# Kernel tuning notes

Hardware: AMD Instinct MI355X
Metric: run time of the kernel (lower is better)

The kernel has to match this reference:

```python
import jax, jax.numpy as jnp
import numpy as np

N = 50000  # nodes


def gcn_layer(x, src, dst, W, b):
    """DGL GraphConv with norm='both': D_in^{-1/2} A^T D_out^{-1/2} x W + b."""
    E = src.shape[0]
    ones = jnp.ones((E,), dtype=x.dtype)
    deg_out = jax.ops.segment_sum(ones, src, num_segments=N)  # out-degree of src nodes
    deg_in = jax.ops.segment_sum(ones, dst, num_segments=N)   # in-degree of dst nodes
    norm_src = jax.lax.rsqrt(jnp.maximum(deg_out, 1.0))
    norm_dst = jax.lax.rsqrt(jnp.maximum(deg_in, 1.0))
    h = x * norm_src[:, None]
    agg = jax.ops.segment_sum(h[src], dst, num_segments=N)  # [N, in_dim]
    return (agg @ W) * norm_dst[:, None] + b


def encoder(feat, src, dst, W1, b1, W2, b2):
    h = jax.nn.relu(gcn_layer(feat, src, dst, W1, b1))
    h = jax.nn.relu(gcn_layer(h, src, dst, W2, b2))
    return h


def proj(h, fc1_W, fc1_b, fc2_W, fc2_b):
    z = jax.nn.elu(h @ fc1_W + fc1_b)
    return z @ fc2_W + fc2_b


def setup_inputs() -> dict:
    key = jax.random.key(0)
    ks = jax.random.split(key, 12)
    in_dim, hid, out_dim, E = 128, 128, 128, 800000
    inp = {
        "feat1": jax.random.normal(ks[0], (N, in_dim), dtype=jnp.float32),
        "feat2": jax.random.normal(ks[1], (N, in_dim), dtype=jnp.float32),
        "edge_index1": jax.random.randint(ks[2], (2, E), 0, N),
        "edge_index2": jax.random.randint(ks[3], (2, E), 0, N),
        # GraphConv weights: in_dim -> 2*hid -> hid
        "conv1_W": jax.random.normal(ks[4], (in_dim, 2 * hid), dtype=jnp.float32) * 0.05,
        "conv1_b": jnp.zeros((2 * hid,), dtype=jnp.float32),
        "conv2_W": jax.random.normal(ks[5], (2 * hid, hid), dtype=jnp.float32) * 0.05,
        "conv2_b": jnp.zeros((hid,), dtype=jnp.float32),
        # MLP proj: fc1 hid->out, fc2 out->hid
        "fc1_W": jax.random.normal(ks[6], (hid, out_dim), dtype=jnp.float32) * 0.05,
        "fc1_b": jnp.zeros((out_dim,), dtype=jnp.float32),
        "fc2_W": jax.random.normal(ks[7], (out_dim, hid), dtype=jnp.float32) * 0.05,
        "fc2_b": jnp.zeros((hid,), dtype=jnp.float32),
    }
    return inp


def reference(feat1, feat2, edge_index1, edge_index2,
              conv1_W, conv1_b, conv2_W, conv2_b,
              fc1_W, fc1_b, fc2_W, fc2_b):
    h1 = encoder(feat1, edge_index1[0], edge_index1[1], conv1_W, conv1_b, conv2_W, conv2_b)
    h2 = encoder(feat2, edge_index2[0], edge_index2[1], conv1_W, conv1_b, conv2_W, conv2_b)
    z1 = proj(h1, fc1_W, fc1_b, fc2_W, fc2_b)
    z2 = proj(h2, fc1_W, fc1_b, fc2_W, fc2_b)
    return (z1, z2)
```

## Files before the change

### kernel.cpp

```cpp
#include <hip/hip_runtime.h>
#include <math.h>

#define NDIM 128
#define H2   256
#define MAXG 2
#define TPE  8192
#define NBKMAX 512

typedef __attribute__((ext_vector_type(8))) short bf16x8;
typedef __attribute__((ext_vector_type(4))) float f32x4;

__device__ __forceinline__ unsigned short f2bf(float f) {
    unsigned int u = __float_as_uint(f);
    u += 0x7fffu + ((u >> 16) & 1u);
    return (unsigned short)(u >> 16);
}
__device__ __forceinline__ float bf2f(unsigned short h) {
    return __uint_as_float(((unsigned int)h) << 16);
}
__device__ __forceinline__ void split2(float f, unsigned short& h, unsigned short& l) {
    h = f2bf(f);
    l = f2bf(f - bf2f(h));
}

__device__ __forceinline__ void gload16(const unsigned short* g, unsigned short* l) {
    __builtin_amdgcn_global_load_lds(
        (const __attribute__((address_space(1))) unsigned int*)g,
        (__attribute__((address_space(3))) unsigned int*)l, 16, 0, 0);
}

struct BinArgs {
    const int* src[MAXG]; const int* dst[MAXG];
    int* histD[MAXG]; int* histS[MAXG];
    int* totD[MAXG];  int* baseD[MAXG];
    int* totS[MAXG];  int* baseS[MAXG];
    unsigned int* pairs[MAXG];
    unsigned short* srcS[MAXG];
    int E[MAXG]; int NBK; int NT; int n;
};

__global__ __launch_bounds__(256) void binA(BinArgs a) {
    __shared__ int cntD[NBKMAX], cntS[NBKMAX];
    int g = blockIdx.y, t = blockIdx.x, tid = threadIdx.x;
    for (int b = tid; b < NBKMAX; b += 256) { cntD[b] = 0; cntS[b] = 0; }
    __syncthreads();
    int E = a.E[g];
    int base = t * TPE;
#pragma unroll
    for (int k = 0; k < TPE / 256; ++k) {
        int e = base + k * 256 + tid;
        if (e < E) {
            atomicAdd(&cntD[a.dst[g][e] >> 7], 1);
            atomicAdd(&cntS[a.src[g][e] >> 7], 1);
        }
    }
    __syncthreads();
    for (int b = tid; b < a.NBK; b += 256) {
        a.histD[g][t * a.NBK + b] = cntD[b];
        a.histS[g][t * a.NBK + b] = cntS[b];
    }
}

__global__ __launch_bounds__(512) void binB(BinArgs a) {
    int g = blockIdx.y, side = blockIdx.z;
    int* hist = side ? a.histS[g] : a.histD[g];
    int* tot  = side ? a.totS[g]  : a.totD[g];
    int* base = side ? a.baseS[g] : a.baseD[g];
    __shared__ int s[512];
    int b = threadIdx.x;
    int v = 0;
    if (b < a.NBK)
        for (int t = 0; t < a.NT; ++t) v += hist[t * a.NBK + b];
    s[b] = v;
    __syncthreads();
    for (int off = 1; off < 512; off <<= 1) {
        int u = (b >= off) ? s[b - off] : 0;
        __syncthreads();
        s[b] += u;
        __syncthreads();
    }
    int excl = s[b] - v;
    if (b < a.NBK) {
        tot[b] = v;
        base[b] = excl;
        int run = excl;
        for (int t = 0; t < a.NT; ++t) {
            int h = hist[t * a.NBK + b];
            hist[t * a.NBK + b] = run;
            run += h;
        }
    }
}

__global__ __launch_bounds__(256) void binC(BinArgs a) {
    __shared__ int offD[NBKMAX], offS[NBKMAX];
    int g = blockIdx.y, t = blockIdx.x, tid = threadIdx.x;
    for (int b = tid; b < a.NBK; b += 256) {
        offD[b] = a.histD[g][t * a.NBK + b];
        offS[b] = a.histS[g][t * a.NBK + b];
    }
    __syncthreads();
    int E = a.E[g];
    int base = t * TPE;
    unsigned int* pairs = a.pairs[g];
    unsigned short* ss = a.srcS[g];
#pragma unroll
    for (int k = 0; k < TPE / 256; ++k) {
        int e = base + k * 256 + tid;
        if (e < E) {
            int s = a.src[g][e], d = a.dst[g][e];
            int pos = atomicAdd(&offD[d >> 7], 1);
            pairs[pos] = ((unsigned int)(d & 127) << 16) | (unsigned int)s;
            int posS = atomicAdd(&offS[s >> 7], 1);
            ss[posS] = (unsigned short)s;
        }
    }
}

struct FinArgs {
    const unsigned int* pairs[MAXG];
    const unsigned short* srcS[MAXG];
    const int* totD[MAXG]; const int* baseD[MAXG];
    const int* totS[MAXG]; const int* baseS[MAXG];
    int* row_ptr[MAXG]; int* row_end[MAXG];
    unsigned short* edge_srt[MAXG];
    float* ns[MAXG]; float* nd[MAXG];
    int n;
};

__global__ __launch_bounds__(256) void finalize(FinArgs a) {
    __shared__ int cnt[128], hist[128], scn[128], cur[128];
    int g = blockIdx.y, bkt = blockIdx.x, tid = threadIdx.x;
    if (tid < 128) { cnt[tid] = 0; hist[tid] = 0; }
    __syncthreads();
    {
        int base = a.baseS[g][bkt], tot = a.totS[g][bkt];
        const unsigned short* ss = a.srcS[g];
        for (int i = tid; i < tot; i += 256)
            atomicAdd(&cnt[ss[base + i] & 127], 1);
    }
    int cntE = a.totD[g][bkt], base = a.baseD[g][bkt];
    const unsigned int* pp = a.pairs[g] + base;
    for (int i = tid; i < cntE; i += 256)
        atomicAdd(&hist[pp[i] >> 16], 1);
    __syncthreads();
    if (tid < 128) {
        int node = bkt * 128 + tid;
        if (node < a.n) {
            int c = cnt[tid];
            a.ns[g][node] = rsqrtf((float)(c > 1 ? c : 1));
        }
        scn[tid] = hist[tid];
    }
    __syncthreads();
    for (int off = 1; off < 128; off <<= 1) {
        int v = (tid < 128 && tid >= off) ? scn[tid - off] : 0;
        __syncthreads();
        if (tid < 128) scn[tid] += v;
        __syncthreads();
    }
    if (tid < 128) {
        int incl = scn[tid];
        int h = hist[tid];
        cur[tid] = incl - h;
        int node = bkt * 128 + tid;
        if (node < a.n) {
            a.row_ptr[g][node] = base + incl - h;
            a.row_end[g][node] = base + incl;
            a.nd[g][node] = rsqrtf((float)(h > 1 ? h : 1));
        }
    }
    __syncthreads();
    for (int i = tid; i < cntE; i += 256) {
        unsigned int p = pp[i];
        int pos = atomicAdd(&cur[p >> 16], 1);
        a.edge_srt[g][base + pos] = (unsigned short)(p & 0xFFFF);
    }
}

struct GatherArgs {
    const float* X[MAXG];
    const int* row_ptr[MAXG]; const int* row_end[MAXG];
    const unsigned short* edge_src[MAXG];
    const float* nd[MAXG];
    const float* sns[MAXG];
    unsigned short* outH[MAXG]; unsigned short* outL[MAXG];
    const float* bias; int use_nd; int use_sns; int n;
};

__global__ __launch_bounds__(256) void gather_split_b(GatherArgs a) {
    int g = blockIdx.y;
    int half = threadIdx.x >> 5;
    int lane = threadIdx.x & 31;
    int r = blockIdx.x * 8 + half;
    if (r >= a.n) return;
    int j = a.row_ptr[g][r];
    int end = a.row_end[g][r];
    const unsigned short* ep = a.edge_src[g];
    const float* X = a.X[g];
    const float* sns = a.sns[g];
    int base = lane * 4;
    float4 acc = make_float4(0.f, 0.f, 0.f, 0.f);
    if (a.use_sns) {
        for (; j + 3 < end; j += 4) {
            int s0 = ep[j], s1 = ep[j + 1], s2 = ep[j + 2], s3 = ep[j + 3];
            float n0 = sns[s0], n1 = sns[s1], n2 = sns[s2], n3 = sns[s3];
            float4 v0 = *(const float4*)(X + (size_t)s0 * NDIM + base);
            float4 v1 = *(const float4*)(X + (size_t)s1 * NDIM + base);
            float4 v2 = *(const float4*)(X + (size_t)s2 * NDIM + base);
            float4 v3 = *(const float4*)(X + (size_t)s3 * NDIM + base);
            acc.x = fmaf(v0.x, n0, fmaf(v1.x, n1, fmaf(v2.x, n2, fmaf(v3.x, n3, acc.x))));
            acc.y = fmaf(v0.y, n0, fmaf(v1.y, n1, fmaf(v2.y, n2, fmaf(v3.y, n3, acc.y))));
            acc.z = fmaf(v0.z, n0, fmaf(v1.z, n1, fmaf(v2.z, n2, fmaf(v3.z, n3, acc.z))));
            acc.w = fmaf(v0.w, n0, fmaf(v1.w, n1, fmaf(v2.w, n2, fmaf(v3.w, n3, acc.w))));
        }
        for (; j < end; ++j) {
            int s0 = ep[j];
            float n0 = sns[s0];
            float4 v0 = *(const float4*)(X + (size_t)s0 * NDIM + base);
            acc.x = fmaf(v0.x, n0, acc.x); acc.y = fmaf(v0.y, n0, acc.y);
            acc.z = fmaf(v0.z, n0, acc.z); acc.w = fmaf(v0.w, n0, acc.w);
        }
    } else {
        for (; j + 3 < end; j += 4) {
            int s0 = ep[j], s1 = ep[j + 1], s2 = ep[j + 2], s3 = ep[j + 3];
            float4 v0 = *(const float4*)(X + (size_t)s0 * NDIM + base);
            float4 v1 = *(const float4*)(X + (size_t)s1 * NDIM + base);
            float4 v2 = *(const float4*)(X + (size_t)s2 * NDIM + base);
            float4 v3 = *(const float4*)(X + (size_t)s3 * NDIM + base);
            acc.x += v0.x + v1.x + v2.x + v3.x;
            acc.y += v0.y + v1.y + v2.y + v3.y;
            acc.z += v0.z + v1.z + v2.z + v3.z;
            acc.w += v0.w + v1.w + v2.w + v3.w;
        }
        for (; j < end; ++j) {
            int s0 = ep[j];
            float4 v0 = *(const float4*)(X + (size_t)s0 * NDIM + base);
            acc.x += v0.x; acc.y += v0.y; acc.z += v0.z; acc.w += v0.w;
        }
    }
    float v[4] = {acc.x, acc.y, acc.z, acc.w};
    if (a.use_nd) {
        float s = a.nd[g][r];
#pragma unroll
        for (int i = 0; i < 4; ++i)
            v[i] = fmaxf(v[i] * s + a.bias[base + i], 0.f);
    }
    unsigned short h[4], l[4];
#pragma unroll
    for (int i = 0; i < 4; ++i) split2(v[i], h[i], l[i]);
    *(ushort4*)(a.outH[g] + (size_t)r * NDIM + base) = make_ushort4(h[0], h[1], h[2], h[3]);
    *(ushort4*)(a.outL[g] + (size_t)r * NDIM + base) = make_ushort4(l[0], l[1], l[2], l[3]);
}

__global__ void wprep_all(const float* __restrict__ W1, const float* __restrict__ W2,
                          const float* __restrict__ F1, const float* __restrict__ F2,
                          unsigned short* __restrict__ W1h, unsigned short* __restrict__ W1l,
                          unsigned short* __restrict__ W2h, unsigned short* __restrict__ W2l,
                          unsigned short* __restrict__ F1h, unsigned short* __restrict__ F1l,
                          unsigned short* __restrict__ F2h, unsigned short* __restrict__ F2l) {
    int i = blockIdx.x * 256 + threadIdx.x;
    const float* Wsrc; unsigned short *Hd, *Ld; int K, Nc, idx;
    if (i < 32768)       { Wsrc = W1; Hd = W1h; Ld = W1l; K = 128; Nc = 256; idx = i; }
    else if (i < 65536)  { Wsrc = W2; Hd = W2h; Ld = W2l; K = 256; Nc = 128; idx = i - 32768; }
    else if (i < 81920)  { Wsrc = F1; Hd = F1h; Ld = F1l; K = 128; Nc = 128; idx = i - 65536; }
    else                 { Wsrc = F2; Hd = F2h; Ld = F2l; K = 128; Nc = 128; idx = i - 81920; }
    int k = idx / Nc, n = idx % Nc;
    unsigned short h, l;
    split2(Wsrc[idx], h, l);
    Hd[n * K + k] = h;
    Ld[n * K + k] = l;
}

struct FusedArgs {
    const unsigned short* Ah[MAXG]; const unsigned short* Al[MAXG];
    const unsigned short* B1h; const unsigned short* B1l;
    const unsigned short* B2h; const unsigned short* B2l;
    const float* rs1[MAXG];
    const float* rs2[MAXG];
    const float* b1v;
    const float* b2v;
    float* C[MAXG];
    int M, has_rs1, has_rs2, has_b1, has_b2;
};

template <int K1, int N1, int ACT1, int ROWS>
__global__ __launch_bounds__(256) void fused_gemm2(FusedArgs a) {
    constexpr int IR   = ROWS / 16;
    constexpr int SH_A = ROWS * K1;
    constexpr int SH_X = ROWS * N1;
    constexpr int SH   = (2 * SH_A > 2 * SH_X) ? 2 * SH_A : 2 * SH_X;
    __shared__ __align__(16) unsigned short S[SH];
    unsigned short* As_h = S;
    unsigned short* As_l = S + SH_A;
    unsigned short* Xs_h = S;
    unsigned short* Xs_l = S + SH_X;

    int g = blockIdx.y;
    const unsigned short* __restrict__ Ah_g = a.Ah[g];
    const unsigned short* __restrict__ Al_g = a.Al[g];
    const unsigned short* __restrict__ B1h = a.B1h;
    const unsigned short* __restrict__ B1l = a.B1l;
    const unsigned short* __restrict__ B2h = a.B2h;
    const unsigned short* __restrict__ B2l = a.B2l;

    int tid  = threadIdx.x;
    int wave = tid >> 6, lane = tid & 63;
    int quad = lane >> 4, l16 = lane & 15;
    int rowBase = blockIdx.x * ROWS;
    int M = a.M;

    constexpr int J1  = N1 / 64;
    constexpr int KT1 = K1 / 32;
    constexpr int KT2 = N1 / 32;
    int wcol1 = wave * (N1 / 4);
    int wcol2 = wave * 32;

    size_t b1off[J1];
#pragma unroll
    for (int j = 0; j < J1; ++j)
        b1off[j] = (size_t)(wcol1 + j * 16 + l16) * K1 + quad * 8;
    size_t b2off[2];
#pragma unroll
    for (int j = 0; j < 2; ++j)
        b2off[j] = (size_t)(wcol2 + j * 16 + l16) * N1 + quad * 8;

    auto loadB1 = [&](int kt, bf16x8 (&bh)[J1], bf16x8 (&bl)[J1]) {
#pragma unroll
        for (int j = 0; j < J1; ++j) {
            bh[j] = *(const bf16x8*)(B1h + b1off[j] + kt * 32);
            bl[j] = *(const bf16x8*)(B1l + b1off[j] + kt * 32);
        }
    };
    auto loadB2 = [&](int kt, bf16x8 (&bh)[2], bf16x8 (&bl)[2]) {
#pragma unroll
        for (int j = 0; j < 2; ++j) {
            bh[j] = *(const bf16x8*)(B2h + b2off[j] + kt * 32);
            bl[j] = *(const bf16x8*)(B2l + b2off[j] + kt * 32);
        }
    };

    bf16x8 b1hA[J1], b1lA[J1], b1hB[J1], b1lB[J1];
    loadB1(0, b1hA, b1lA);

    constexpr int CPR = K1 / 8;
#pragma unroll
    for (int it = 0; it < (ROWS * CPR) / 256; ++it) {
        int waveChunk = it * 256 + wave * 64;
        int cl   = waveChunk + lane;
        int row  = cl / CPR;
        int cpos = cl % CPR;
        int oc   = cpos ^ (row & 7);
        int grow = rowBase + row; if (grow > M - 1) grow = M - 1;
        gload16(Ah_g + (size_t)grow * K1 + oc * 8, As_h + (size_t)waveChunk * 8);
        gload16(Al_g + (size_t)grow * K1 + oc * 8, As_l + (size_t)waveChunk * 8);
    }
    __syncthreads();

    f32x4 acc1[IR][J1] = {};
    auto stepP1 = [&](int kt, bf16x8 (&bh)[J1], bf16x8 (&bl)[J1]) {
        bf16x8 af[IR], alf[IR];
#pragma unroll
        for (int i = 0; i < IR; ++i) {
            int r  = i * 16 + l16;
            int sc = (kt * 4 + quad) ^ (r & 7);
            af[i]  = *(const bf16x8*)(As_h + r * K1 + sc * 8);
            alf[i] = *(const bf16x8*)(As_l + r * K1 + sc * 8);
        }
#pragma unroll
        for (int i = 0; i < IR; ++i)
#pragma unroll
            for (int j = 0; j < J1; ++j) {
                acc1[i][j] = __builtin_amdgcn_mfma_f32_16x16x32_bf16(af[i],  bh[j], acc1[i][j], 0, 0, 0);
                acc1[i][j] = __builtin_amdgcn_mfma_f32_16x16x32_bf16(alf[i], bh[j], acc1[i][j], 0, 0, 0);
                acc1[i][j] = __builtin_amdgcn_mfma_f32_16x16x32_bf16(af[i],  bl[j], acc1[i][j], 0, 0, 0);
            }
    };
#pragma unroll
    for (int kt = 0; kt < KT1; kt += 2) {
        if (kt + 1 < KT1) loadB1(kt + 1, b1hB, b1lB);
        stepP1(kt, b1hA, b1lA);
        if (kt + 2 < KT1) loadB1(kt + 2, b1hA, b1lA);
        if (kt + 1 < KT1) stepP1(kt + 1, b1hB, b1lB);
    }

    bf16x8 b2hA[2], b2lA[2], b2hB[2], b2lB[2];
    loadB2(0, b2hA, b2lA);

    __syncthreads();

    const float* rs1p = a.has_rs1 ? a.rs1[g] : nullptr;
#pragma unroll
    for (int i = 0; i < IR; ++i) {
#pragma unroll
        for (int rr = 0; rr < 4; ++rr) {
            int row  = i * 16 + quad * 4 + rr;
            int grow = rowBase + row;
            float rs = 1.0f;
            if (rs1p) rs = (grow < M) ? rs1p[grow] : 0.0f;
#pragma unroll
            for (int j = 0; j < J1; ++j) {
                int col = wcol1 + j * 16 + l16;
                float v = acc1[i][j][rr] * rs;
                if (a.has_b1) v += a.b1v[col];
                if (ACT1 == 1) v = fmaxf(v, 0.f);
                else           v = v > 0.f ? v : expm1f(v);
                unsigned short h, l;
                split2(v, h, l);
                int oc = col >> 3, within = col & 7;
                int sc = oc ^ (row & 7);
                Xs_h[row * N1 + sc * 8 + within] = h;
                Xs_l[row * N1 + sc * 8 + within] = l;
            }
        }
    }
    __syncthreads();

    f32x4 acc2[IR][2] = {};
    auto stepP2 = [&](int kt, bf16x8 (&bh)[2], bf16x8 (&bl)[2]) {
        bf16x8 xf[IR], xlf[IR];
#pragma unroll
        for (int i = 0; i < IR; ++i) {
            int r  = i * 16 + l16;
            int sc = (kt * 4 + quad) ^ (r & 7);
            xf[i]  = *(const bf16x8*)(Xs_h + r * N1 + sc * 8);
            xlf[i] = *(const bf16x8*)(Xs_l + r * N1 + sc * 8);
        }
#pragma unroll
        for (int i = 0; i < IR; ++i)
#pragma unroll
            for (int j = 0; j < 2; ++j) {
                acc2[i][j] = __builtin_amdgcn_mfma_f32_16x16x32_bf16(xf[i],  bh[j], acc2[i][j], 0, 0, 0);
                acc2[i][j] = __builtin_amdgcn_mfma_f32_16x16x32_bf16(xlf[i], bh[j], acc2[i][j], 0, 0, 0);
                acc2[i][j] = __builtin_amdgcn_mfma_f32_16x16x32_bf16(xf[i],  bl[j], acc2[i][j], 0, 0, 0);
            }
    };
#pragma unroll
    for (int kt = 0; kt < KT2; kt += 2) {
        if (kt + 1 < KT2) loadB2(kt + 1, b2hB, b2lB);
        stepP2(kt, b2hA, b2lA);
        if (kt + 2 < KT2) loadB2(kt + 2, b2hA, b2lA);
        if (kt + 1 < KT2) stepP2(kt + 1, b2hB, b2lB);
    }

    const float* rs2p = a.has_rs2 ? a.rs2[g] : nullptr;
#pragma unroll
    for (int i = 0; i < IR; ++i) {
#pragma unroll
        for (int rr = 0; rr < 4; ++rr) {
            int grow = rowBase + i * 16 + quad * 4 + rr;
            if (grow >= M) continue;
            float rs = rs2p ? rs2p[grow] : 1.0f;
#pragma unroll
            for (int j = 0; j < 2; ++j) {
                int col = wcol2 + j * 16 + l16;
                float v = acc2[i][j][rr] * rs;
                if (a.has_b2) v += a.b2v[col];
                a.C[g][(size_t)grow * NDIM + col] = v;
            }
        }
    }
}

extern "C" void kernel_launch(void* const* d_in, const int* in_sizes, int n_in,
                              void* d_out, int out_size, void* d_ws, size_t ws_size,
                              hipStream_t stream) {
    const float* feat[2] = {(const float*)d_in[0], (const float*)d_in[1]};
    const int*   ei[2]   = {(const int*)d_in[2], (const int*)d_in[3]};
    const float* W1   = (const float*)d_in[4];
    const float* b1   = (const float*)d_in[5];
    const float* W2   = (const float*)d_in[6];
    const float* b2   = (const float*)d_in[7];
    const float* fc1W = (const float*)d_in[8];
    const float* fc1b = (const float*)d_in[9];
    const float* fc2W = (const float*)d_in[10];
    const float* fc2b = (const float*)d_in[11];
    int N = in_sizes[0] / NDIM;
    float* out = (float*)d_out;

    int Emax = 0;
    for (int g = 0; g < 2; ++g) { int E = in_sizes[2 + g] / 2; if (E > Emax) Emax = E; }
    int NBK = (N + 127) / 128;
    int NT  = (Emax + TPE - 1) / TPE;

    char* p = (char*)d_ws;
    float* ns_[2]; float* nd_[2];
    for (int i = 0; i < 2; ++i) { ns_[i] = (float*)p; p += (size_t)N * 4; }
    for (int i = 0; i < 2; ++i) { nd_[i] = (float*)p; p += (size_t)N * 4; }
    int* rp_[2]; int* re_[2]; unsigned short* esrt_[2];
    for (int i = 0; i < 2; ++i) { rp_[i] = (int*)p; p += (size_t)N * 4; }
    for (int i = 0; i < 2; ++i) { re_[i] = (int*)p; p += (size_t)N * 4; }
    for (int i = 0; i < 2; ++i) { esrt_[i] = (unsigned short*)p; p += (size_t)Emax * 2; }
    unsigned short* R1[2]; unsigned short* R2[2];
    for (int i = 0; i < 2; ++i) { R1[i] = (unsigned short*)p; p += (size_t)N * NDIM * 2 * 2; }
    for (int i = 0; i < 2; ++i) { R2[i] = (unsigned short*)p; p += (size_t)N * H2 * 2 * 2; }
    unsigned short* W1th = (unsigned short*)p; p += (size_t)NDIM * H2 * 2;
    unsigned short* W1tl = (unsigned short*)p; p += (size_t)NDIM * H2 * 2;
    unsigned short* W2th = (unsigned short*)p; p += (size_t)H2 * NDIM * 2;
    unsigned short* W2tl = (unsigned short*)p; p += (size_t)H2 * NDIM * 2;
    unsigned short* f1th = (unsigned short*)p; p += (size_t)NDIM * NDIM * 2;
    unsigned short* f1tl = (unsigned short*)p; p += (size_t)NDIM * NDIM * 2;
    unsigned short* f2th = (unsigned short*)p; p += (size_t)NDIM * NDIM * 2;
    unsigned short* f2tl = (unsigned short*)p; p += (size_t)NDIM * NDIM * 2;
    int* tb = (int*)p; p += (size_t)2 * 4 * NBK * 4;

    int* histD_[2]; int* histS_[2]; unsigned int* pairs_[2]; unsigned short* srcS_[2];
    for (int i = 0; i < 2; ++i) {
        histD_[i] = (int*)R2[i];
        histS_[i] = (int*)R2[i] + (size_t)NT * NBK;
        pairs_[i] = (unsigned int*)((char*)R2[i] + (1 << 20));
        srcS_[i]  = (unsigned short*)R1[i];
    }

    BinArgs ba = {};
    ba.NBK = NBK; ba.NT = NT; ba.n = N;
    for (int i = 0; i < 2; ++i) {
        int E = in_sizes[2 + i] / 2;
        ba.src[i] = ei[i]; ba.dst[i] = ei[i] + E; ba.E[i] = E;
        ba.histD[i] = histD_[i]; ba.histS[i] = histS_[i];
        ba.totD[i]  = tb + (size_t)i * 4 * NBK;
        ba.baseD[i] = tb + (size_t)i * 4 * NBK + NBK;
        ba.totS[i]  = tb + (size_t)i * 4 * NBK + 2 * NBK;
        ba.baseS[i] = tb + (size_t)i * 4 * NBK + 3 * NBK;
        ba.pairs[i] = pairs_[i]; ba.srcS[i] = srcS_[i];
    }

    wprep_all<<<384, 256, 0, stream>>>(W1, W2, fc1W, fc2W,
                                       W1th, W1tl, W2th, W2tl, f1th, f1tl, f2th, f2tl);
    binA<<<dim3(NT, 2), 256, 0, stream>>>(ba);
    binB<<<dim3(1, 2, 2), 512, 0, stream>>>(ba);
    binC<<<dim3(NT, 2), 256, 0, stream>>>(ba);

    FinArgs fa = {};
    fa.n = N;
    for (int i = 0; i < 2; ++i) {
        fa.pairs[i] = pairs_[i]; fa.srcS[i] = srcS_[i];
        fa.totD[i] = ba.totD[i]; fa.baseD[i] = ba.baseD[i];
        fa.totS[i] = ba.totS[i]; fa.baseS[i] = ba.baseS[i];
        fa.row_ptr[i] = rp_[i]; fa.row_end[i] = re_[i];
        fa.edge_srt[i] = esrt_[i];
        fa.ns[i] = ns_[i]; fa.nd[i] = nd_[i];
    }
    finalize<<<dim3(NBK, 2), 256, 0, stream>>>(fa);

    unsigned short *A1h[2], *A1l[2], *Gh[2], *Gl[2];
    float* T[2];
    for (int i = 0; i < 2; ++i) {
        A1h[i] = R1[i]; A1l[i] = R1[i] + (size_t)N * NDIM;
        T[i]   = (float*)R2[i];
        Gh[i]  = R2[i] + (size_t)N * 256;
        Gl[i]  = R2[i] + (size_t)N * 256 + (size_t)N * NDIM;
    }

    int ggrid = (N + 7) / 8;
    int mgrid = (N + 63) / 64;

    GatherArgs ga = {};
    ga.n = N; ga.use_nd = 0; ga.use_sns = 1; ga.bias = b2;
    for (int i = 0; i < 2; ++i) {
        ga.X[i] = feat[i];
        ga.row_ptr[i] = rp_[i]; ga.row_end[i] = re_[i]; ga.edge_src[i] = esrt_[i];
        ga.nd[i] = nd_[i]; ga.sns[i] = ns_[i];
        ga.outH[i] = A1h[i]; ga.outL[i] = A1l[i];
    }
    gather_split_b<<<dim3(ggrid, 2), 256, 0, stream>>>(ga);

    FusedArgs f12 = {};
    f12.B1h = W1th; f12.B1l = W1tl; f12.B2h = W2th; f12.B2l = W2tl;
    f12.b1v = b1; f12.has_b1 = 1; f12.has_b2 = 0;
    f12.has_rs1 = 1; f12.has_rs2 = 1;
    f12.M = N;
    for (int i = 0; i < 2; ++i) {
        f12.Ah[i] = A1h[i]; f12.Al[i] = A1l[i];
        f12.rs1[i] = nd_[i]; f12.rs2[i] = ns_[i];
        f12.C[i] = T[i];
    }
    fused_gemm2<128, 256, 1, 64><<<dim3(mgrid, 2), 256, 0, stream>>>(f12);

    GatherArgs gb = ga;
    gb.use_nd = 1; gb.use_sns = 0;
    for (int i = 0; i < 2; ++i) {
        gb.X[i] = T[i];
        gb.outH[i] = Gh[i]; gb.outL[i] = Gl[i];
    }
    gather_split_b<<<dim3(ggrid, 2), 256, 0, stream>>>(gb);

    FusedArgs f34 = {};
    f34.B1h = f1th; f34.B1l = f1tl; f34.B2h = f2th; f34.B2l = f2tl;
    f34.b1v = fc1b; f34.has_b1 = 1; f34.b2v = fc2b; f34.has_b2 = 1;
    f34.has_rs1 = 0; f34.has_rs2 = 0;
    f34.M = N;
    for (int i = 0; i < 2; ++i) {
        f34.Ah[i] = Gh[i]; f34.Al[i] = Gl[i];
        f34.C[i] = out + (size_t)i * N * NDIM;
    }
    fused_gemm2<128, 128, 2, 64><<<dim3(mgrid, 2), 256, 0, stream>>>(f34);
}
```

Before: 589.9 us.

## Fuse sparse gather aggregation into fused GEMM kernels with 512-thread blocks

The separate gather kernels are removed. Each fused GEMM kernel now does the neighbour aggregation for its 64-row tile itself and writes the bf16 hi/lo split straight into swizzled LDS. This drops the global round trip of the split activations and two kernel launches. Blocks grow to 512 threads (8 waves), each wave taking half as many output columns. The gather phase now sits inside a GEMM block with large LDS use, which may reduce occupancy while the latency-bound gather runs.

```diff
diff --git a/kernel.cpp b/kernel.cpp
--- a/kernel.cpp
+++ b/kernel.cpp
@@ -21,12 +21,6 @@
 __device__ __forceinline__ void split2(float f, unsigned short& h, unsigned short& l) {
     h = f2bf(f);
     l = f2bf(f - bf2f(h));
-}
-
-__device__ __forceinline__ void gload16(const unsigned short* g, unsigned short* l) {
-    __builtin_amdgcn_global_load_lds(
-        (const __attribute__((address_space(1))) unsigned int*)g,
-        (__attribute__((address_space(3))) unsigned int*)l, 16, 0, 0);
 }
 
 struct BinArgs {
@@ -176,81 +170,6 @@
         int pos = atomicAdd(&cur[p >> 16], 1);
         a.edge_srt[g][base + pos] = (unsigned short)(p & 0xFFFF);
     }
-}
-
-struct GatherArgs {
-    const float* X[MAXG];
-    const int* row_ptr[MAXG]; const int* row_end[MAXG];
-    const unsigned short* edge_src[MAXG];
-    const float* nd[MAXG];
-    const float* sns[MAXG];
-    unsigned short* outH[MAXG]; unsigned short* outL[MAXG];
-    const float* bias; int use_nd; int use_sns; int n;
-};
-
-__global__ __launch_bounds__(256) void gather_split_b(GatherArgs a) {
-    int g = blockIdx.y;
-    int half = threadIdx.x >> 5;
-    int lane = threadIdx.x & 31;
-    int r = blockIdx.x * 8 + half;
-    if (r >= a.n) return;
-    int j = a.row_ptr[g][r];
-    int end = a.row_end[g][r];
-    const unsigned short* ep = a.edge_src[g];
-    const float* X = a.X[g];
-    const float* sns = a.sns[g];
-    int base = lane * 4;
-    float4 acc = make_float4(0.f, 0.f, 0.f, 0.f);
-    if (a.use_sns) {
-        for (; j + 3 < end; j += 4) {
-            int s0 = ep[j], s1 = ep[j + 1], s2 = ep[j + 2], s3 = ep[j + 3];
-            float n0 = sns[s0], n1 = sns[s1], n2 = sns[s2], n3 = sns[s3];
-            float4 v0 = *(const float4*)(X + (size_t)s0 * NDIM + base);
-            float4 v1 = *(const float4*)(X + (size_t)s1 * NDIM + base);
-            float4 v2 = *(const float4*)(X + (size_t)s2 * NDIM + base);
-            float4 v3 = *(const float4*)(X + (size_t)s3 * NDIM + base);
-            acc.x = fmaf(v0.x, n0, fmaf(v1.x, n1, fmaf(v2.x, n2, fmaf(v3.x, n3, acc.x))));
-            acc.y = fmaf(v0.y, n0, fmaf(v1.y, n1, fmaf(v2.y, n2, fmaf(v3.y, n3, acc.y))));
-            acc.z = fmaf(v0.z, n0, fmaf(v1.z, n1, fmaf(v2.z, n2, fmaf(v3.z, n3, acc.z))));
-            acc.w = fmaf(v0.w, n0, fmaf(v1.w, n1, fmaf(v2.w, n2, fmaf(v3.w, n3, acc.w))));
-        }
-        for (; j < end; ++j) {
-            int s0 = ep[j];
-            float n0 = sns[s0];
-            float4 v0 = *(const float4*)(X + (size_t)s0 * NDIM + base);
-            acc.x = fmaf(v0.x, n0, acc.x); acc.y = fmaf(v0.y, n0, acc.y);
-            acc.z = fmaf(v0.z, n0, acc.z); acc.w = fmaf(v0.w, n0, acc.w);
-        }
-    } else {
-        for (; j + 3 < end; j += 4) {
-            int s0 = ep[j], s1 = ep[j + 1], s2 = ep[j + 2], s3 = ep[j + 3];
-            float4 v0 = *(const float4*)(X + (size_t)s0 * NDIM + base);
-            float4 v1 = *(const float4*)(X + (size_t)s1 * NDIM + base);
-            float4 v2 = *(const float4*)(X + (size_t)s2 * NDIM + base);
-            float4 v3 = *(const float4*)(X + (size_t)s3 * NDIM + base);
-            acc.x += v0.x + v1.x + v2.x + v3.x;
-            acc.y += v0.y + v1.y + v2.y + v3.y;
-            acc.z += v0.z + v1.z + v2.z + v3.z;
-            acc.w += v0.w + v1.w + v2.w + v3.w;
-        }
-        for (; j < end; ++j) {
-            int s0 = ep[j];
-            float4 v0 = *(const float4*)(X + (size_t)s0 * NDIM + base);
-            acc.x += v0.x; acc.y += v0.y; acc.z += v0.z; acc.w += v0.w;
-        }
-    }
-    float v[4] = {acc.x, acc.y, acc.z, acc.w};
-    if (a.use_nd) {
-        float s = a.nd[g][r];
-#pragma unroll
-        for (int i = 0; i < 4; ++i)
-            v[i] = fmaxf(v[i] * s + a.bias[base + i], 0.f);
-    }
-    unsigned short h[4], l[4];
-#pragma unroll
-    for (int i = 0; i < 4; ++i) split2(v[i], h[i], l[i]);
-    *(ushort4*)(a.outH[g] + (size_t)r * NDIM + base) = make_ushort4(h[0], h[1], h[2], h[3]);
-    *(ushort4*)(a.outL[g] + (size_t)r * NDIM + base) = make_ushort4(l[0], l[1], l[2], l[3]);
 }
 
 __global__ void wprep_all(const float* __restrict__ W1, const float* __restrict__ W2,
@@ -273,19 +192,22 @@
 }
 
 struct FusedArgs {
-    const unsigned short* Ah[MAXG]; const unsigned short* Al[MAXG];
+    const float* Xg[MAXG];
+    const int* rp[MAXG]; const int* re[MAXG];
+    const unsigned short* ep[MAXG];
+    const float* sns[MAXG];
+    const float* ndv[MAXG];
+    const float* gbias;
     const unsigned short* B1h; const unsigned short* B1l;
     const unsigned short* B2h; const unsigned short* B2l;
-    const float* rs1[MAXG];
-    const float* rs2[MAXG];
-    const float* b1v;
-    const float* b2v;
+    const float* rs1[MAXG]; const float* rs2[MAXG];
+    const float* b1v; const float* b2v;
     float* C[MAXG];
     int M, has_rs1, has_rs2, has_b1, has_b2;
 };
 
-template <int K1, int N1, int ACT1, int ROWS>
-__global__ __launch_bounds__(256) void fused_gemm2(FusedArgs a) {
+template <int K1, int N1, int ACT1, int ROWS, int GMODE>
+__global__ __launch_bounds__(512, 4) void fused_g(FusedArgs a) {
     constexpr int IR   = ROWS / 16;
     constexpr int SH_A = ROWS * K1;
     constexpr int SH_X = ROWS * N1;
@@ -297,8 +219,6 @@
     unsigned short* Xs_l = S + SH_X;
 
     int g = blockIdx.y;
-    const unsigned short* __restrict__ Ah_g = a.Ah[g];
-    const unsigned short* __restrict__ Al_g = a.Al[g];
     const unsigned short* __restrict__ B1h = a.B1h;
     const unsigned short* __restrict__ B1l = a.B1l;
     const unsigned short* __restrict__ B2h = a.B2h;
@@ -310,20 +230,87 @@
     int rowBase = blockIdx.x * ROWS;
     int M = a.M;
 
-    constexpr int J1  = N1 / 64;
+    {
+        int half  = tid >> 5;
+        int glane = tid & 31;
+        const float* X   = a.Xg[g];
+        const float* sns = a.sns[g];
+        const unsigned short* ep = a.ep[g];
+        int base = glane * 4;
+#pragma unroll
+        for (int ps = 0; ps < ROWS / 16; ++ps) {
+            int row  = ps * 16 + half;
+            int grow = rowBase + row;
+            float4 acc = make_float4(0.f, 0.f, 0.f, 0.f);
+            if (grow < M) {
+                int j = a.rp[g][grow], end = a.re[g][grow];
+                if (GMODE == 1) {
+                    for (; j + 3 < end; j += 4) {
+                        int s0 = ep[j], s1 = ep[j + 1], s2 = ep[j + 2], s3 = ep[j + 3];
+                        float n0 = sns[s0], n1 = sns[s1], n2 = sns[s2], n3 = sns[s3];
+                        float4 v0 = *(const float4*)(X + (size_t)s0 * NDIM + base);
+                        float4 v1 = *(const float4*)(X + (size_t)s1 * NDIM + base);
+                        float4 v2 = *(const float4*)(X + (size_t)s2 * NDIM + base);
+                        float4 v3 = *(const float4*)(X + (size_t)s3 * NDIM + base);
+                        acc.x = fmaf(v0.x, n0, fmaf(v1.x, n1, fmaf(v2.x, n2, fmaf(v3.x, n3, acc.x))));
+                        acc.y = fmaf(v0.y, n0, fmaf(v1.y, n1, fmaf(v2.y, n2, fmaf(v3.y, n3, acc.y))));
+                        acc.z = fmaf(v0.z, n0, fmaf(v1.z, n1, fmaf(v2.z, n2, fmaf(v3.z, n3, acc.z))));
+                        acc.w = fmaf(v0.w, n0, fmaf(v1.w, n1, fmaf(v2.w, n2, fmaf(v3.w, n3, acc.w))));
+                    }
+                    for (; j < end; ++j) {
+                        int s0 = ep[j];
+                        float n0 = sns[s0];
+                        float4 v0 = *(const float4*)(X + (size_t)s0 * NDIM + base);
+                        acc.x = fmaf(v0.x, n0, acc.x); acc.y = fmaf(v0.y, n0, acc.y);
+                        acc.z = fmaf(v0.z, n0, acc.z); acc.w = fmaf(v0.w, n0, acc.w);
+                    }
+                } else {
+                    for (; j + 3 < end; j += 4) {
+                        int s0 = ep[j], s1 = ep[j + 1], s2 = ep[j + 2], s3 = ep[j + 3];
+                        float4 v0 = *(const float4*)(X + (size_t)s0 * NDIM + base);
+                        float4 v1 = *(const float4*)(X + (size_t)s1 * NDIM + base);
+                        float4 v2 = *(const float4*)(X + (size_t)s2 * NDIM + base);
+                        float4 v3 = *(const float4*)(X + (size_t)s3 * NDIM + base);
+                        acc.x += v0.x + v1.x + v2.x + v3.x;
+                        acc.y += v0.y + v1.y + v2.y + v3.y;
+                        acc.z += v0.z + v1.z + v2.z + v3.z;
+                        acc.w += v0.w + v1.w + v2.w + v3.w;
+                    }
+                    for (; j < end; ++j) {
+                        int s0 = ep[j];
+                        float4 v0 = *(const float4*)(X + (size_t)s0 * NDIM + base);
+                        acc.x += v0.x; acc.y += v0.y; acc.z += v0.z; acc.w += v0.w;
+                    }
+                }
+            }
+            float v[4] = {acc.x, acc.y, acc.z, acc.w};
+            if (GMODE == 2) {
+                float s = (grow < M) ? a.ndv[g][grow] : 0.f;
+#pragma unroll
+                for (int c = 0; c < 4; ++c)
+                    v[c] = fmaxf(v[c] * s + a.gbias[base + c], 0.f);
+            }
+            unsigned short h[4], l[4];
+#pragma unroll
+            for (int c = 0; c < 4; ++c) split2(v[c], h[c], l[c]);
+            int oc = glane >> 1, within = (glane & 1) * 4;
+            int sc = oc ^ (row & 7);
+            *(ushort4*)(As_h + row * K1 + sc * 8 + within) = make_ushort4(h[0], h[1], h[2], h[3]);
+            *(ushort4*)(As_l + row * K1 + sc * 8 + within) = make_ushort4(l[0], l[1], l[2], l[3]);
+        }
+    }
+
+    constexpr int J1  = N1 / 128;
     constexpr int KT1 = K1 / 32;
     constexpr int KT2 = N1 / 32;
-    int wcol1 = wave * (N1 / 4);
-    int wcol2 = wave * 32;
+    int wcol1 = wave * (N1 / 8);
+    int wcol2 = wave * 16;
 
     size_t b1off[J1];
 #pragma unroll
     for (int j = 0; j < J1; ++j)
         b1off[j] = (size_t)(wcol1 + j * 16 + l16) * K1 + quad * 8;
-    size_t b2off[2];
-#pragma unroll
-    for (int j = 0; j < 2; ++j)
-        b2off[j] = (size_t)(wcol2 + j * 16 + l16) * N1 + quad * 8;
+    size_t b2off = (size_t)(wcol2 + l16) * N1 + quad * 8;
 
     auto loadB1 = [&](int kt, bf16x8 (&bh)[J1], bf16x8 (&bl)[J1]) {
 #pragma unroll
@@ -332,29 +319,13 @@
             bl[j] = *(const bf16x8*)(B1l + b1off[j] + kt * 32);
         }
     };
-    auto loadB2 = [&](int kt, bf16x8 (&bh)[2], bf16x8 (&bl)[2]) {
-#pragma unroll
-        for (int j = 0; j < 2; ++j) {
-            bh[j] = *(const bf16x8*)(B2h + b2off[j] + kt * 32);
-            bl[j] = *(const bf16x8*)(B2l + b2off[j] + kt * 32);
-        }
+    auto loadB2 = [&](int kt, bf16x8 (&bh)[1], bf16x8 (&bl)[1]) {
+        bh[0] = *(const bf16x8*)(B2h + b2off + kt * 32);
+        bl[0] = *(const bf16x8*)(B2l + b2off + kt * 32);
     };
 
     bf16x8 b1hA[J1], b1lA[J1], b1hB[J1], b1lB[J1];
     loadB1(0, b1hA, b1lA);
-
-    constexpr int CPR = K1 / 8;
-#pragma unroll
-    for (int it = 0; it < (ROWS * CPR) / 256; ++it) {
-        int waveChunk = it * 256 + wave * 64;
-        int cl   = waveChunk + lane;
-        int row  = cl / CPR;
-        int cpos = cl % CPR;
-        int oc   = cpos ^ (row & 7);
-        int grow = rowBase + row; if (grow > M - 1) grow = M - 1;
-        gload16(Ah_g + (size_t)grow * K1 + oc * 8, As_h + (size_t)waveChunk * 8);
-        gload16(Al_g + (size_t)grow * K1 + oc * 8, As_l + (size_t)waveChunk * 8);
-    }
     __syncthreads();
 
     f32x4 acc1[IR][J1] = {};
@@ -384,7 +355,7 @@
         if (kt + 1 < KT1) stepP1(kt + 1, b1hB, b1lB);
     }
 
-    bf16x8 b2hA[2], b2lA[2], b2hB[2], b2lB[2];
+    bf16x8 b2hA[1], b2lA[1], b2hB[1], b2lB[1];
     loadB2(0, b2hA, b2lA);
 
     __syncthreads();
@@ -416,8 +387,8 @@
     }
     __syncthreads();
 
-    f32x4 acc2[IR][2] = {};
-    auto stepP2 = [&](int kt, bf16x8 (&bh)[2], bf16x8 (&bl)[2]) {
+    f32x4 acc2[IR][1] = {};
+    auto stepP2 = [&](int kt, bf16x8 (&bh)[1], bf16x8 (&bl)[1]) {
         bf16x8 xf[IR], xlf[IR];
 #pragma unroll
         for (int i = 0; i < IR; ++i) {
@@ -427,13 +398,11 @@
             xlf[i] = *(const bf16x8*)(Xs_l + r * N1 + sc * 8);
         }
 #pragma unroll
-        for (int i = 0; i < IR; ++i)
-#pragma unroll
-            for (int j = 0; j < 2; ++j) {
-                acc2[i][j] = __builtin_amdgcn_mfma_f32_16x16x32_bf16(xf[i],  bh[j], acc2[i][j], 0, 0, 0);
-                acc2[i][j] = __builtin_amdgcn_mfma_f32_16x16x32_bf16(xlf[i], bh[j], acc2[i][j], 0, 0, 0);
-                acc2[i][j] = __builtin_amdgcn_mfma_f32_16x16x32_bf16(xf[i],  bl[j], acc2[i][j], 0, 0, 0);
-            }
+        for (int i = 0; i < IR; ++i) {
+            acc2[i][0] = __builtin_amdgcn_mfma_f32_16x16x32_bf16(xf[i],  bh[0], acc2[i][0], 0, 0, 0);
+            acc2[i][0] = __builtin_amdgcn_mfma_f32_16x16x32_bf16(xlf[i], bh[0], acc2[i][0], 0, 0, 0);
+            acc2[i][0] = __builtin_amdgcn_mfma_f32_16x16x32_bf16(xf[i],  bl[0], acc2[i][0], 0, 0, 0);
+        }
     };
 #pragma unroll
     for (int kt = 0; kt < KT2; kt += 2) {
@@ -451,13 +420,10 @@
             int grow = rowBase + i * 16 + quad * 4 + rr;
             if (grow >= M) continue;
             float rs = rs2p ? rs2p[grow] : 1.0f;
-#pragma unroll
-            for (int j = 0; j < 2; ++j) {
-                int col = wcol2 + j * 16 + l16;
-                float v = acc2[i][j][rr] * rs;
-                if (a.has_b2) v += a.b2v[col];
-                a.C[g][(size_t)grow * NDIM + col] = v;
-            }
+            int col = wcol2 + l16;
+            float v = acc2[i][0][rr] * rs;
+            if (a.has_b2) v += a.b2v[col];
+            a.C[g][(size_t)grow * NDIM + col] = v;
         }
     }
 }
@@ -543,27 +509,11 @@
     }
     finalize<<<dim3(NBK, 2), 256, 0, stream>>>(fa);
 
-    unsigned short *A1h[2], *A1l[2], *Gh[2], *Gl[2];
     float* T[2];
-    for (int i = 0; i < 2; ++i) {
-        A1h[i] = R1[i]; A1l[i] = R1[i] + (size_t)N * NDIM;
-        T[i]   = (float*)R2[i];
-        Gh[i]  = R2[i] + (size_t)N * 256;
-        Gl[i]  = R2[i] + (size_t)N * 256 + (size_t)N * NDIM;
-    }
-
-    int ggrid = (N + 7) / 8;
+    for (int i = 0; i < 2; ++i)
+        T[i] = (float*)R2[i];
+
     int mgrid = (N + 63) / 64;
-
-    GatherArgs ga = {};
-    ga.n = N; ga.use_nd = 0; ga.use_sns = 1; ga.bias = b2;
-    for (int i = 0; i < 2; ++i) {
-        ga.X[i] = feat[i];
-        ga.row_ptr[i] = rp_[i]; ga.row_end[i] = re_[i]; ga.edge_src[i] = esrt_[i];
-        ga.nd[i] = nd_[i]; ga.sns[i] = ns_[i];
-        ga.outH[i] = A1h[i]; ga.outL[i] = A1l[i];
-    }
-    gather_split_b<<<dim3(ggrid, 2), 256, 0, stream>>>(ga);
 
     FusedArgs f12 = {};
     f12.B1h = W1th; f12.B1l = W1tl; f12.B2h = W2th; f12.B2l = W2tl;
@@ -571,28 +521,25 @@
     f12.has_rs1 = 1; f12.has_rs2 = 1;
     f12.M = N;
     for (int i = 0; i < 2; ++i) {
-        f12.Ah[i] = A1h[i]; f12.Al[i] = A1l[i];
+        f12.Xg[i] = feat[i];
+        f12.rp[i] = rp_[i]; f12.re[i] = re_[i]; f12.ep[i] = esrt_[i];
+        f12.sns[i] = ns_[i]; f12.ndv[i] = nd_[i];
         f12.rs1[i] = nd_[i]; f12.rs2[i] = ns_[i];
         f12.C[i] = T[i];
     }
-    fused_gemm2<128, 256, 1, 64><<<dim3(mgrid, 2), 256, 0, stream>>>(f12);
-
-    GatherArgs gb = ga;
-    gb.use_nd = 1; gb.use_sns = 0;
-    for (int i = 0; i < 2; ++i) {
-        gb.X[i] = T[i];
-        gb.outH[i] = Gh[i]; gb.outL[i] = Gl[i];
-    }
-    gather_split_b<<<dim3(ggrid, 2), 256, 0, stream>>>(gb);
+    fused_g<128, 256, 1, 64, 1><<<dim3(mgrid, 2), 512, 0, stream>>>(f12);
 
     FusedArgs f34 = {};
     f34.B1h = f1th; f34.B1l = f1tl; f34.B2h = f2th; f34.B2l = f2tl;
     f34.b1v = fc1b; f34.has_b1 = 1; f34.b2v = fc2b; f34.has_b2 = 1;
     f34.has_rs1 = 0; f34.has_rs2 = 0;
+    f34.gbias = b2;
     f34.M = N;
     for (int i = 0; i < 2; ++i) {
-        f34.Ah[i] = Gh[i]; f34.Al[i] = Gl[i];
+        f34.Xg[i] = T[i];
+        f34.rp[i] = rp_[i]; f34.re[i] = re_[i]; f34.ep[i] = esrt_[i];
+        f34.sns[i] = ns_[i]; f34.ndv[i] = nd_[i];
         f34.C[i] = out + (size_t)i * N * NDIM;
     }
-    fused_gemm2<128, 128, 2, 64><<<dim3(mgrid, 2), 256, 0, stream>>>(f34);
-}
+    fused_g<128, 128, 2, 64, 2><<<dim3(mgrid, 2), 512, 0, stream>>>(f34);
+}
```

Measured after the change: 569.7 us. 1.04x faster.
